# Performance work log

Measured on AMD Instinct MI355X. Metric: run time of the kernel, lower is better.

Reference implementation:

```python
import jax, jax.numpy as jnp
import numpy as np

SEQ = 4096
D = 1024


def setup_inputs() -> dict:
    key = jax.random.key(0)
    kx, kq, kk, kv = jax.random.split(key, 4)
    x = jax.random.normal(kx, (SEQ, D), dtype=jnp.float32)
    W_Q = jax.random.normal(kq, (D, D), dtype=jnp.float32)
    W_K = jax.random.normal(kk, (D, D), dtype=jnp.float32)
    W_V = jax.random.normal(kv, (D, D), dtype=jnp.float32)
    b_Q = jnp.zeros((D,), dtype=jnp.float32)
    b_K = jnp.zeros((D,), dtype=jnp.float32)
    b_V = jnp.zeros((D,), dtype=jnp.float32)
    return {"x": x, "W_Q": W_Q, "W_K": W_K, "W_V": W_V,
            "b_Q": b_Q, "b_K": b_K, "b_V": b_V}


def reference(x, W_Q, W_K, W_V, b_Q, b_K, b_V):
    d_head = W_Q.shape[0]
    q = x @ W_Q + b_Q                      # [S, D]
    k = x @ W_K + b_K                      # [S, D]
    v = x @ W_V + b_V                      # [S, D]
    scores = (q @ k.T) / jnp.sqrt(jnp.float32(d_head))  # [S, S]
    probs = jax.nn.softmax(scores, axis=-1)              # softmax over last axis
    return probs @ v                        # [S, D]
```

## Files before the change

### kernel.cpp

```cpp
#include <hip/hip_runtime.h>
#include <hip/hip_bf16.h>
#include <stdint.h>

#define SEQLEN 4096
#define DMODEL 1024

typedef uint16_t u16;
typedef uint32_t u32;

typedef __bf16 bf16x8 __attribute__((ext_vector_type(8)));
typedef float  f32x4  __attribute__((ext_vector_type(4)));
typedef u16    u16x8  __attribute__((ext_vector_type(8)));
typedef u16    u16x4  __attribute__((ext_vector_type(4)));

__device__ __forceinline__ u16 f2bf(float f) {
  union { float f; u32 u; } a; a.f = f;
  return (u16)((a.u + 0x7FFFu + ((a.u >> 16) & 1u)) >> 16);
}
__device__ __forceinline__ float bf2f(u16 h) {
  union { u32 u; float f; } a; a.u = ((u32)h) << 16;
  return a.f;
}

__device__ __forceinline__ void gl_lds16(const u16* g, u16* l) {
  __builtin_amdgcn_global_load_lds(
      (const __attribute__((address_space(1))) void*)g,
      (__attribute__((address_space(3))) void*)l,
      16, 0, 0);
}

__device__ __forceinline__ void stage64(const u16* __restrict__ g, int ld,
                                        int row0, int k0, u16* lds, int tid) {
#pragma unroll
  for (int it = 0; it < 4; ++it) {
    int u = tid + 256 * it;
    int row = u >> 3;
    int cg = (u & 7) ^ (row & 7);
    gl_lds16(g + (size_t)(row0 + row) * ld + (size_t)(k0 + cg * 8), lds + u * 8);
  }
}
__device__ __forceinline__ void stage32(const u16* __restrict__ g, int ld,
                                        int row0, int k0, u16* lds, int tid) {
#pragma unroll
  for (int it = 0; it < 2; ++it) {
    int u = tid + 256 * it;
    int row = u >> 2;
    int cg = (u & 3) ^ ((row >> 1) & 3);
    gl_lds16(g + (size_t)(row0 + row) * ld + (size_t)(k0 + cg * 8), lds + u * 8);
  }
}
__device__ __forceinline__ bf16x8 frag64(const u16* lds, int row, int chunk) {
  return *(const bf16x8*)(lds + row * 64 + ((chunk ^ (row & 7)) << 3));
}
__device__ __forceinline__ bf16x8 frag32(const u16* lds, int row, int chunk) {
  return *(const bf16x8*)(lds + row * 32 + ((chunk ^ ((row >> 1) & 3)) << 3));
}

#define MFMA16(c, a, b) c = __builtin_amdgcn_mfma_f32_16x16x32_bf16(a, b, c, 0, 0, 0)

__global__ void split_x_kernel(const float* __restrict__ x,
                               u16* __restrict__ xh, u16* __restrict__ xl) {
  const int total = SEQLEN * DMODEL / 4;
  for (int idx = blockIdx.x * 256 + threadIdx.x; idx < total; idx += gridDim.x * 256) {
    float4 f = ((const float4*)x)[idx];
    float ff[4] = {f.x, f.y, f.z, f.w};
    union { u16x4 v; u16 s[4]; } h, l;
#pragma unroll
    for (int uu = 0; uu < 4; ++uu) {
      u16 hi = f2bf(ff[uu]);
      h.s[uu] = hi;
      l.s[uu] = f2bf(ff[uu] - bf2f(hi));
    }
    ((u16x4*)xh)[idx] = h.v;
    ((u16x4*)xl)[idx] = l.v;
  }
}

__global__ void transpose_w_kernel(const float* __restrict__ W,
                                   u16* __restrict__ wth, u16* __restrict__ wtl) {
  __shared__ float tile[64][65];
  int n0 = (blockIdx.x & 15) * 64;
  int k0 = (blockIdx.x >> 4) * 64;
  int c = threadIdx.x & 63, r0 = threadIdx.x >> 6;
#pragma unroll
  for (int rr = 0; rr < 16; ++rr) {
    int r = r0 * 16 + rr;
    tile[r][c] = W[(size_t)(k0 + r) * DMODEL + n0 + c];
  }
  __syncthreads();
#pragma unroll
  for (int rr = 0; rr < 16; ++rr) {
    int n = r0 * 16 + rr;
    float f = tile[c][n];
    u16 hi = f2bf(f);
    wth[(size_t)(n0 + n) * DMODEL + k0 + c] = hi;
    wtl[(size_t)(n0 + n) * DMODEL + k0 + c] = f2bf(f - bf2f(hi));
  }
}

template <bool THREE, bool SPLITOUT>
__global__ __launch_bounds__(256, 2) void proj_kernel(
    const u16* __restrict__ Ah, const u16* __restrict__ Al,
    const u16* __restrict__ Bh, const u16* __restrict__ Bl,
    const float* __restrict__ bias, float scale,
    u16* __restrict__ outh, u16* __restrict__ outl, u16* __restrict__ outT) {
  __shared__ __align__(16) u16 st[32768];

  int tid = threadIdx.x;
  int lane = tid & 63, wid = tid >> 6;
  int wr = (wid >> 1) * 64, wc = (wid & 1) * 64;
  int r = lane & 15, g = lane >> 4;
  int m0 = blockIdx.x * 128, n0 = blockIdx.y * 128;

  f32x4 acc[4][4];
#pragma unroll
  for (int i = 0; i < 4; ++i)
#pragma unroll
    for (int j = 0; j < 4; ++j) acc[i][j] = (f32x4){0.f, 0.f, 0.f, 0.f};

  if (THREE) {
    stage32(Ah, DMODEL, m0, 0, st + 0 * 4096, tid);
    stage32(Al, DMODEL, m0, 0, st + 1 * 4096, tid);
    stage32(Bh, DMODEL, n0, 0, st + 2 * 4096, tid);
    stage32(Bl, DMODEL, n0, 0, st + 3 * 4096, tid);
    __syncthreads();
    int c = 0;
    for (int step = 0; step < DMODEL / 32; ++step) {
      if (step + 1 < DMODEL / 32) {
        int k0 = (step + 1) * 32;
        u16* nb = st + (c ^ 1) * 16384;
        stage32(Ah, DMODEL, m0, k0, nb + 0 * 4096, tid);
        stage32(Al, DMODEL, m0, k0, nb + 1 * 4096, tid);
        stage32(Bh, DMODEL, n0, k0, nb + 2 * 4096, tid);
        stage32(Bl, DMODEL, n0, k0, nb + 3 * 4096, tid);
      }
      const u16* cb = st + c * 16384;
      bf16x8 fa[4], fb[4], fal[4], fbl[4];
#pragma unroll
      for (int i = 0; i < 4; ++i) {
        fa[i]  = frag32(cb + 0 * 4096, wr + i * 16 + r, g);
        fal[i] = frag32(cb + 1 * 4096, wr + i * 16 + r, g);
        fb[i]  = frag32(cb + 2 * 4096, wc + i * 16 + r, g);
        fbl[i] = frag32(cb + 3 * 4096, wc + i * 16 + r, g);
      }
#pragma unroll
      for (int i = 0; i < 4; ++i)
#pragma unroll
        for (int j = 0; j < 4; ++j) {
          MFMA16(acc[i][j], fa[i], fb[j]);
          MFMA16(acc[i][j], fa[i], fbl[j]);
          MFMA16(acc[i][j], fal[i], fb[j]);
        }
      __syncthreads();
      c ^= 1;
    }
  } else {
    stage64(Ah, DMODEL, m0, 0, st + 0 * 8192, tid);
    stage64(Bh, DMODEL, n0, 0, st + 1 * 8192, tid);
    __syncthreads();
    int c = 0;
    for (int step = 0; step < DMODEL / 64; ++step) {
      if (step + 1 < DMODEL / 64) {
        int k0 = (step + 1) * 64;
        u16* nb = st + (c ^ 1) * 16384;
        stage64(Ah, DMODEL, m0, k0, nb + 0 * 8192, tid);
        stage64(Bh, DMODEL, n0, k0, nb + 1 * 8192, tid);
      }
      const u16* cb = st + c * 16384;
#pragma unroll
      for (int ks = 0; ks < 2; ++ks) {
        bf16x8 fa[4], fb[4];
#pragma unroll
        for (int i = 0; i < 4; ++i) {
          fa[i] = frag64(cb + 0 * 8192, wr + i * 16 + r, ks * 4 + g);
          fb[i] = frag64(cb + 1 * 8192, wc + i * 16 + r, ks * 4 + g);
        }
#pragma unroll
        for (int i = 0; i < 4; ++i)
#pragma unroll
          for (int j = 0; j < 4; ++j) MFMA16(acc[i][j], fa[i], fb[j]);
      }
      __syncthreads();
      c ^= 1;
    }
  }

#pragma unroll
  for (int i = 0; i < 4; ++i)
#pragma unroll
    for (int j = 0; j < 4; ++j) {
      int col = n0 + wc + j * 16 + r;
      float bv = bias[col];
#pragma unroll
      for (int t = 0; t < 4; ++t) {
        int row = m0 + wr + i * 16 + g * 4 + t;
        float v = (acc[i][j][t] + bv) * scale;
        if (SPLITOUT) {
          u16 hi = f2bf(v);
          outh[(size_t)row * DMODEL + col] = hi;
          outl[(size_t)row * DMODEL + col] = f2bf(v - bf2f(hi));
        } else {
          outT[(size_t)col * SEQLEN + row] = f2bf(v);
        }
      }
    }
}

__global__ __launch_bounds__(256, 2) void scores_kernel(
    const u16* __restrict__ qh, const u16* __restrict__ ql,
    const u16* __restrict__ kh, const u16* __restrict__ kl,
    u16* __restrict__ P, float* __restrict__ mloc, float* __restrict__ tsum) {
  __shared__ __align__(16) char smem[128 * 129 * 4];
  u16* st = (u16*)smem;
  float* sS = (float*)smem;

  int tid = threadIdx.x;
  int lane = tid & 63, wid = tid >> 6;
  int wr = (wid >> 1) * 64, wc = (wid & 1) * 64;
  int r = lane & 15, g = lane >> 4;
  int m0 = blockIdx.x * 128, n0 = blockIdx.y * 128;

  f32x4 acc[4][4];
#pragma unroll
  for (int i = 0; i < 4; ++i)
#pragma unroll
    for (int j = 0; j < 4; ++j) acc[i][j] = (f32x4){0.f, 0.f, 0.f, 0.f};

  stage32(qh, DMODEL, m0, 0, st + 0 * 4096, tid);
  stage32(ql, DMODEL, m0, 0, st + 1 * 4096, tid);
  stage32(kh, DMODEL, n0, 0, st + 2 * 4096, tid);
  stage32(kl, DMODEL, n0, 0, st + 3 * 4096, tid);
  __syncthreads();
  int c = 0;
  for (int step = 0; step < DMODEL / 32; ++step) {
    if (step + 1 < DMODEL / 32) {
      int k0 = (step + 1) * 32;
      u16* nb = st + (c ^ 1) * 16384;
      stage32(qh, DMODEL, m0, k0, nb + 0 * 4096, tid);
      stage32(ql, DMODEL, m0, k0, nb + 1 * 4096, tid);
      stage32(kh, DMODEL, n0, k0, nb + 2 * 4096, tid);
      stage32(kl, DMODEL, n0, k0, nb + 3 * 4096, tid);
    }
    const u16* cb = st + c * 16384;
    bf16x8 fa[4], fb[4], fal[4], fbl[4];
#pragma unroll
    for (int i = 0; i < 4; ++i) {
      fa[i]  = frag32(cb + 0 * 4096, wr + i * 16 + r, g);
      fal[i] = frag32(cb + 1 * 4096, wr + i * 16 + r, g);
      fb[i]  = frag32(cb + 2 * 4096, wc + i * 16 + r, g);
      fbl[i] = frag32(cb + 3 * 4096, wc + i * 16 + r, g);
    }
#pragma unroll
    for (int i = 0; i < 4; ++i)
#pragma unroll
      for (int j = 0; j < 4; ++j) {
        MFMA16(acc[i][j], fa[i], fb[j]);
        MFMA16(acc[i][j], fa[i], fbl[j]);
        MFMA16(acc[i][j], fal[i], fb[j]);
      }
    __syncthreads();
    c ^= 1;
  }

#pragma unroll
  for (int i = 0; i < 4; ++i)
#pragma unroll
    for (int j = 0; j < 4; ++j)
#pragma unroll
      for (int t = 0; t < 4; ++t)
        sS[(wr + i * 16 + g * 4 + t) * 129 + wc + j * 16 + r] = acc[i][j][t];
  __syncthreads();

  int rt = tid >> 1, h = tid & 1;
  const float* rowp = sS + rt * 129 + h * 64;
  float mx = -3.0e38f;
#pragma unroll 16
  for (int cc = 0; cc < 64; ++cc) mx = fmaxf(mx, rowp[cc]);
  mx = fmaxf(mx, __shfl_xor(mx, 1));

  float ssum = 0.f;
  int grow = m0 + rt;
  u16* pout = P + (size_t)grow * SEQLEN + n0 + h * 64;
#pragma unroll
  for (int c8 = 0; c8 < 8; ++c8) {
    union { u16 s[8]; u16x8 v; } tmp;
#pragma unroll
    for (int uu = 0; uu < 8; ++uu) {
      float e = exp2f((rowp[c8 * 8 + uu] - mx) * 1.4426950408889634f);
      ssum += e;
      tmp.s[uu] = f2bf(e);
    }
    *(u16x8*)(pout + c8 * 8) = tmp.v;
  }
  ssum += __shfl_xor(ssum, 1);
  if (h == 0) {
    mloc[(size_t)blockIdx.y * SEQLEN + grow] = mx;
    tsum[(size_t)blockIdx.y * SEQLEN + grow] = ssum;
  }
}

__global__ void finalize_kernel(const float* __restrict__ mloc,
                                const float* __restrict__ tsum,
                                float* __restrict__ rowscale) {
  int rr = blockIdx.x * 256 + threadIdx.x;
  if (rr >= SEQLEN) return;
  float M = -3.0e38f;
#pragma unroll
  for (int t = 0; t < 32; ++t) M = fmaxf(M, mloc[t * SEQLEN + rr]);
  float l = 0.f;
#pragma unroll
  for (int t = 0; t < 32; ++t)
    l += tsum[t * SEQLEN + rr] * exp2f((mloc[t * SEQLEN + rr] - M) * 1.4426950408889634f);
  float inv = 1.0f / l;
#pragma unroll
  for (int t = 0; t < 32; ++t)
    rowscale[t * SEQLEN + rr] = exp2f((mloc[t * SEQLEN + rr] - M) * 1.4426950408889634f) * inv;
}

__global__ void pnorm_kernel(u16* __restrict__ P, const float* __restrict__ rowscale) {
  const int total = SEQLEN * SEQLEN / 8;
  for (int idx = blockIdx.x * 256 + threadIdx.x; idx < total; idx += gridDim.x * 256) {
    int rrow = idx >> 9;
    int c8 = idx & 511;
    int t = c8 >> 4;
    float sc = rowscale[t * SEQLEN + rrow];
    union { u16x8 v; u16 s[8]; } d;
    d.v = ((u16x8*)P)[idx];
#pragma unroll
    for (int uu = 0; uu < 8; ++uu) d.s[uu] = f2bf(bf2f(d.s[uu]) * sc);
    ((u16x8*)P)[idx] = d.v;
  }
}

__global__ __launch_bounds__(256, 2) void pv_kernel(const u16* __restrict__ P,
                                                    const u16* __restrict__ vT,
                                                    float* __restrict__ out) {
  __shared__ __align__(16) u16 st[32768];
  int tid = threadIdx.x;
  int lane = tid & 63, wid = tid >> 6;
  int wr = (wid >> 1) * 64, wc = (wid & 1) * 64;
  int r = lane & 15, g = lane >> 4;
  int m0 = blockIdx.x * 128, n0 = blockIdx.y * 128;

  f32x4 acc[4][4];
#pragma unroll
  for (int i = 0; i < 4; ++i)
#pragma unroll
    for (int j = 0; j < 4; ++j) acc[i][j] = (f32x4){0.f, 0.f, 0.f, 0.f};

  stage64(P, SEQLEN, m0, 0, st + 0 * 8192, tid);
  stage64(vT, SEQLEN, n0, 0, st + 1 * 8192, tid);
  __syncthreads();
  int c = 0;
  for (int step = 0; step < SEQLEN / 64; ++step) {
    if (step + 1 < SEQLEN / 64) {
      int k0 = (step + 1) * 64;
      u16* nb = st + (c ^ 1) * 16384;
      stage64(P, SEQLEN, m0, k0, nb + 0 * 8192, tid);
      stage64(vT, SEQLEN, n0, k0, nb + 1 * 8192, tid);
    }
    const u16* cb = st + c * 16384;
#pragma unroll
    for (int ks = 0; ks < 2; ++ks) {
      bf16x8 fa[4], fb[4];
#pragma unroll
      for (int i = 0; i < 4; ++i) {
        fa[i] = frag64(cb + 0 * 8192, wr + i * 16 + r, ks * 4 + g);
        fb[i] = frag64(cb + 1 * 8192, wc + i * 16 + r, ks * 4 + g);
      }
#pragma unroll
      for (int i = 0; i < 4; ++i)
#pragma unroll
        for (int j = 0; j < 4; ++j) MFMA16(acc[i][j], fa[i], fb[j]);
    }
    __syncthreads();
    c ^= 1;
  }
#pragma unroll
  for (int i = 0; i < 4; ++i)
#pragma unroll
    for (int j = 0; j < 4; ++j)
#pragma unroll
      for (int t = 0; t < 4; ++t)
        out[(size_t)(m0 + wr + i * 16 + g * 4 + t) * DMODEL + n0 + wc + j * 16 + r] =
            acc[i][j][t];
}

extern "C" void kernel_launch(void* const* d_in, const int* in_sizes, int n_in,
                              void* d_out, int out_size, void* d_ws, size_t ws_size,
                              hipStream_t stream) {
  (void)in_sizes; (void)n_in; (void)out_size; (void)ws_size;
  const float* x  = (const float*)d_in[0];
  const float* WQ = (const float*)d_in[1];
  const float* WK = (const float*)d_in[2];
  const float* WV = (const float*)d_in[3];
  const float* bQ = (const float*)d_in[4];
  const float* bK = (const float*)d_in[5];
  const float* bV = (const float*)d_in[6];
  float* out = (float*)d_out;
  char* ws = (char*)d_ws;
  const size_t MB = 1ull << 20;

  u16* xh   = (u16*)(ws + 0);
  u16* xl   = (u16*)(ws + 8 * MB);
  u16* wqh  = (u16*)(ws + 16 * MB);
  u16* wql  = (u16*)(ws + 18 * MB);
  u16* wkh  = (u16*)(ws + 20 * MB);
  u16* wkl  = (u16*)(ws + 22 * MB);
  u16* wvh  = (u16*)(ws + 24 * MB);
  u16* wvl  = (u16*)(ws + 26 * MB);
  u16* P    = (u16*)(ws + 0);
  u16* qh   = (u16*)(ws + 32 * MB);
  u16* ql   = (u16*)(ws + 40 * MB);
  u16* kh   = (u16*)(ws + 48 * MB);
  u16* kl   = (u16*)(ws + 56 * MB);
  u16* vT   = (u16*)(ws + 64 * MB);
  float* mloc     = (float*)(ws + 72 * MB);
  float* tsum     = (float*)(ws + 72 * MB + 512 * 1024);
  float* rowscale = (float*)(ws + 73 * MB);

  split_x_kernel<<<2048, 256, 0, stream>>>(x, xh, xl);
  transpose_w_kernel<<<256, 256, 0, stream>>>(WQ, wqh, wql);
  transpose_w_kernel<<<256, 256, 0, stream>>>(WK, wkh, wkl);
  transpose_w_kernel<<<256, 256, 0, stream>>>(WV, wvh, wvl);

  dim3 gproj(32, 8);
  proj_kernel<true, true><<<gproj, 256, 0, stream>>>(xh, xl, wqh, wql, bQ,
                                                     1.0f / 32.0f, qh, ql, nullptr);
  proj_kernel<true, true><<<gproj, 256, 0, stream>>>(xh, xl, wkh, wkl, bK,
                                                     1.0f, kh, kl, nullptr);
  proj_kernel<false, false><<<gproj, 256, 0, stream>>>(xh, nullptr, wvh, nullptr, bV,
                                                       1.0f, nullptr, nullptr, vT);

  dim3 gsc(32, 32);
  scores_kernel<<<gsc, 256, 0, stream>>>(qh, ql, kh, kl, P, mloc, tsum);
  finalize_kernel<<<16, 256, 0, stream>>>(mloc, tsum, rowscale);
  pnorm_kernel<<<4096, 256, 0, stream>>>(P, rowscale);

  dim3 gpv(32, 8);
  pv_kernel<<<gpv, 256, 0, stream>>>(P, vT, out);
}
```

Measured before the change: 337.8 us.

## Deepen LDS prefetch to two tiles ahead with explicit vmcnt waits

All four GEMM main loops now issue global-to-LDS loads two K-tiles ahead instead of one. They use a partial `s_waitcnt vmcnt(8)` plus a raw barrier in place of `__syncthreads`, which drains every outstanding load. This keeps more memory traffic in flight while the MFMAs run, aiming to hide load latency. It relies on hand-counted vmcnt values matching the number of loads each stage issues, which is fragile if the staging helpers change.

```diff
diff --git a/kernel.cpp b/kernel.cpp
--- a/kernel.cpp
+++ b/kernel.cpp
@@ -12,6 +12,10 @@
 typedef float  f32x4  __attribute__((ext_vector_type(4)));
 typedef u16    u16x8  __attribute__((ext_vector_type(8)));
 typedef u16    u16x4  __attribute__((ext_vector_type(4)));
+
+#define VMCNT8() asm volatile("s_waitcnt vmcnt(8)" ::: "memory")
+#define VMCNT0() asm volatile("s_waitcnt vmcnt(0)" ::: "memory")
+#define BAR() __builtin_amdgcn_s_barrier()
 
 __device__ __forceinline__ u16 f2bf(float f) {
   union { float f; u32 u; } a; a.f = f;
@@ -119,22 +123,19 @@
     for (int j = 0; j < 4; ++j) acc[i][j] = (f32x4){0.f, 0.f, 0.f, 0.f};
 
   if (THREE) {
+    const int NT = DMODEL / 32;
     stage32(Ah, DMODEL, m0, 0, st + 0 * 4096, tid);
     stage32(Al, DMODEL, m0, 0, st + 1 * 4096, tid);
     stage32(Bh, DMODEL, n0, 0, st + 2 * 4096, tid);
     stage32(Bl, DMODEL, n0, 0, st + 3 * 4096, tid);
-    __syncthreads();
-    int c = 0;
-    for (int step = 0; step < DMODEL / 32; ++step) {
-      if (step + 1 < DMODEL / 32) {
-        int k0 = (step + 1) * 32;
-        u16* nb = st + (c ^ 1) * 16384;
-        stage32(Ah, DMODEL, m0, k0, nb + 0 * 4096, tid);
-        stage32(Al, DMODEL, m0, k0, nb + 1 * 4096, tid);
-        stage32(Bh, DMODEL, n0, k0, nb + 2 * 4096, tid);
-        stage32(Bl, DMODEL, n0, k0, nb + 3 * 4096, tid);
-      }
-      const u16* cb = st + c * 16384;
+    stage32(Ah, DMODEL, m0, 32, st + 16384 + 0 * 4096, tid);
+    stage32(Al, DMODEL, m0, 32, st + 16384 + 1 * 4096, tid);
+    stage32(Bh, DMODEL, n0, 32, st + 16384 + 2 * 4096, tid);
+    stage32(Bl, DMODEL, n0, 32, st + 16384 + 3 * 4096, tid);
+    for (int t = 0; t < NT; ++t) {
+      if (t < NT - 1) VMCNT8(); else VMCNT0();
+      BAR();
+      const u16* cb = st + (t & 1) * 16384;
       bf16x8 fa[4], fb[4], fal[4], fbl[4];
 #pragma unroll
       for (int i = 0; i < 4; ++i) {
@@ -151,22 +152,26 @@
           MFMA16(acc[i][j], fa[i], fbl[j]);
           MFMA16(acc[i][j], fal[i], fb[j]);
         }
-      __syncthreads();
-      c ^= 1;
+      BAR();
+      if (t + 2 < NT) {
+        int k0 = (t + 2) * 32;
+        u16* nb = st + (t & 1) * 16384;
+        stage32(Ah, DMODEL, m0, k0, nb + 0 * 4096, tid);
+        stage32(Al, DMODEL, m0, k0, nb + 1 * 4096, tid);
+        stage32(Bh, DMODEL, n0, k0, nb + 2 * 4096, tid);
+        stage32(Bl, DMODEL, n0, k0, nb + 3 * 4096, tid);
+      }
     }
   } else {
+    const int NT = DMODEL / 64;
     stage64(Ah, DMODEL, m0, 0, st + 0 * 8192, tid);
     stage64(Bh, DMODEL, n0, 0, st + 1 * 8192, tid);
-    __syncthreads();
-    int c = 0;
-    for (int step = 0; step < DMODEL / 64; ++step) {
-      if (step + 1 < DMODEL / 64) {
-        int k0 = (step + 1) * 64;
-        u16* nb = st + (c ^ 1) * 16384;
-        stage64(Ah, DMODEL, m0, k0, nb + 0 * 8192, tid);
-        stage64(Bh, DMODEL, n0, k0, nb + 1 * 8192, tid);
-      }
-      const u16* cb = st + c * 16384;
+    stage64(Ah, DMODEL, m0, 64, st + 16384 + 0 * 8192, tid);
+    stage64(Bh, DMODEL, n0, 64, st + 16384 + 1 * 8192, tid);
+    for (int t = 0; t < NT; ++t) {
+      if (t < NT - 1) VMCNT8(); else VMCNT0();
+      BAR();
+      const u16* cb = st + (t & 1) * 16384;
 #pragma unroll
       for (int ks = 0; ks < 2; ++ks) {
         bf16x8 fa[4], fb[4];
@@ -180,8 +185,13 @@
 #pragma unroll
           for (int j = 0; j < 4; ++j) MFMA16(acc[i][j], fa[i], fb[j]);
       }
-      __syncthreads();
-      c ^= 1;
+      BAR();
+      if (t + 2 < NT) {
+        int k0 = (t + 2) * 64;
+        u16* nb = st + (t & 1) * 16384;
+        stage64(Ah, DMODEL, m0, k0, nb + 0 * 8192, tid);
+        stage64(Bh, DMODEL, n0, k0, nb + 1 * 8192, tid);
+      }
     }
   }
 
@@ -226,22 +236,19 @@
 #pragma unroll
     for (int j = 0; j < 4; ++j) acc[i][j] = (f32x4){0.f, 0.f, 0.f, 0.f};
 
+  const int NT = DMODEL / 32;
   stage32(qh, DMODEL, m0, 0, st + 0 * 4096, tid);
   stage32(ql, DMODEL, m0, 0, st + 1 * 4096, tid);
   stage32(kh, DMODEL, n0, 0, st + 2 * 4096, tid);
   stage32(kl, DMODEL, n0, 0, st + 3 * 4096, tid);
-  __syncthreads();
-  int c = 0;
-  for (int step = 0; step < DMODEL / 32; ++step) {
-    if (step + 1 < DMODEL / 32) {
-      int k0 = (step + 1) * 32;
-      u16* nb = st + (c ^ 1) * 16384;
-      stage32(qh, DMODEL, m0, k0, nb + 0 * 4096, tid);
-      stage32(ql, DMODEL, m0, k0, nb + 1 * 4096, tid);
-      stage32(kh, DMODEL, n0, k0, nb + 2 * 4096, tid);
-      stage32(kl, DMODEL, n0, k0, nb + 3 * 4096, tid);
-    }
-    const u16* cb = st + c * 16384;
+  stage32(qh, DMODEL, m0, 32, st + 16384 + 0 * 4096, tid);
+  stage32(ql, DMODEL, m0, 32, st + 16384 + 1 * 4096, tid);
+  stage32(kh, DMODEL, n0, 32, st + 16384 + 2 * 4096, tid);
+  stage32(kl, DMODEL, n0, 32, st + 16384 + 3 * 4096, tid);
+  for (int t = 0; t < NT; ++t) {
+    if (t < NT - 1) VMCNT8(); else VMCNT0();
+    BAR();
+    const u16* cb = st + (t & 1) * 16384;
     bf16x8 fa[4], fb[4], fal[4], fbl[4];
 #pragma unroll
     for (int i = 0; i < 4; ++i) {
@@ -258,8 +265,15 @@
         MFMA16(acc[i][j], fa[i], fbl[j]);
         MFMA16(acc[i][j], fal[i], fb[j]);
       }
-    __syncthreads();
-    c ^= 1;
+    BAR();
+    if (t + 2 < NT) {
+      int k0 = (t + 2) * 32;
+      u16* nb = st + (t & 1) * 16384;
+      stage32(qh, DMODEL, m0, k0, nb + 0 * 4096, tid);
+      stage32(ql, DMODEL, m0, k0, nb + 1 * 4096, tid);
+      stage32(kh, DMODEL, n0, k0, nb + 2 * 4096, tid);
+      stage32(kl, DMODEL, n0, k0, nb + 3 * 4096, tid);
+    }
   }
 
 #pragma unroll
@@ -348,18 +362,15 @@
 #pragma unroll
     for (int j = 0; j < 4; ++j) acc[i][j] = (f32x4){0.f, 0.f, 0.f, 0.f};
 
+  const int NT = SEQLEN / 64;
   stage64(P, SEQLEN, m0, 0, st + 0 * 8192, tid);
   stage64(vT, SEQLEN, n0, 0, st + 1 * 8192, tid);
-  __syncthreads();
-  int c = 0;
-  for (int step = 0; step < SEQLEN / 64; ++step) {
-    if (step + 1 < SEQLEN / 64) {
-      int k0 = (step + 1) * 64;
-      u16* nb = st + (c ^ 1) * 16384;
-      stage64(P, SEQLEN, m0, k0, nb + 0 * 8192, tid);
-      stage64(vT, SEQLEN, n0, k0, nb + 1 * 8192, tid);
-    }
-    const u16* cb = st + c * 16384;
+  stage64(P, SEQLEN, m0, 64, st + 16384 + 0 * 8192, tid);
+  stage64(vT, SEQLEN, n0, 64, st + 16384 + 1 * 8192, tid);
+  for (int t = 0; t < NT; ++t) {
+    if (t < NT - 1) VMCNT8(); else VMCNT0();
+    BAR();
+    const u16* cb = st + (t & 1) * 16384;
 #pragma unroll
     for (int ks = 0; ks < 2; ++ks) {
       bf16x8 fa[4], fb[4];
@@ -373,8 +384,13 @@
 #pragma unroll
         for (int j = 0; j < 4; ++j) MFMA16(acc[i][j], fa[i], fb[j]);
     }
-    __syncthreads();
-    c ^= 1;
+    BAR();
+    if (t + 2 < NT) {
+      int k0 = (t + 2) * 64;
+      u16* nb = st + (t & 1) * 16384;
+      stage64(P, SEQLEN, m0, k0, nb + 0 * 8192, tid);
+      stage64(vT, SEQLEN, n0, k0, nb + 1 * 8192, tid);
+    }
   }
 #pragma unroll
   for (int i = 0; i < 4; ++i)
```

Measured after the change: 334.7 us. Within noise of the previous version (-0.9%).
